# Optimization experiments

Hardware: AMD Instinct MI355X
Metric: run time of the kernel (lower is better)

## Reference

```python
import jax, jax.numpy as jnp
import numpy as np

EPS = 1e-5

def mvn(x):
    # instance norm with torch's unbiased variance (ddof=1), eps added to var
    b, c = x.shape[:2]
    flat = x.reshape(b, c, -1)
    mean = flat.mean(axis=2)[:, :, None, None]
    std = jnp.sqrt(flat.var(axis=2, ddof=1) + EPS)[:, :, None, None]
    return (x - mean) / std

def conv1x1(x, w, b):
    # w: [Cout, Cin], b: [Cout], x: [B, Cin, H, W]
    return jnp.einsum('oc,bchw->bohw', w, x) + b[None, :, None, None]

def setup_inputs() -> dict:
    key = jax.random.key(0)
    ks = jax.random.split(key, 20)
    B, C, H, W = 4, 512, 64, 64
    s = 1.0 / np.sqrt(C)  # kaiming-ish scale for stable softmax logits
    inp = {
        'content': jax.random.normal(ks[0], (B, C, H, W), jnp.float32),
        'style':   jax.random.normal(ks[1], (B, C, H, W), jnp.float32),
        'v_w':   jax.random.normal(ks[2], (C, C), jnp.float32) * s,
        'v_b':   jax.random.normal(ks[3], (C,), jnp.float32) * 0.01,
        'vsp_w': jax.random.normal(ks[4], (1, C), jnp.float32) * s,
        'vsp_b': jax.random.normal(ks[5], (1,), jnp.float32) * 0.01,
        'k_w':   jax.random.normal(ks[6], (C, C), jnp.float32) * s,
        'k_b':   jax.random.normal(ks[7], (C,), jnp.float32) * 0.01,
        'qg_w':  jax.random.normal(ks[8], (C, C), jnp.float32) * s,
        'qg_b':  jax.random.normal(ks[9], (C,), jnp.float32) * 0.01,
        'g1_w1': jax.random.normal(ks[10], (C, C), jnp.float32) * s,
        'g1_b1': jax.random.normal(ks[11], (C,), jnp.float32) * 0.01,
        'g1_w2': jax.random.normal(ks[12], (C, C), jnp.float32) * s,
        'g1_b2': jax.random.normal(ks[13], (C,), jnp.float32) * 0.01,
        'g2_w1': jax.random.normal(ks[14], (C, C), jnp.float32) * s,
        'g2_b1': jax.random.normal(ks[15], (C,), jnp.float32) * 0.01,
        'g2_w2': jax.random.normal(ks[16], (C, C), jnp.float32) * s,
        'g2_b2': jax.random.normal(ks[17], (C,), jnp.float32) * 0.01,
    }
    return inp

def reference(content, style, v_w, v_b, vsp_w, vsp_b, k_w, k_b, qg_w, qg_b,
              g1_w1, g1_b1, g1_w2, g1_b2, g2_w1, g2_b1, g2_w2, g2_b2):
    b, c, h_s, w_s = style.shape
    _, _, h_c, w_c = content.shape
    Ls, Lc = h_s * w_s, h_c * w_c

    V = conv1x1(style, v_w, v_b)                                  # [b,c,hs,ws]
    key_pool = conv1x1(mvn(style), vsp_w, vsp_b).reshape(b, 1, Ls)
    style_weights = jax.nn.softmax(key_pool, axis=-1)             # [b,1,Ls]
    # global style vector: V_flat @ weights^T -> [b,c,1]
    gsv = jnp.einsum('bcl,bl->bc', V.reshape(b, c, Ls), style_weights[:, 0, :])
    gsv4 = gsv[:, :, None, None]                                  # [b,c,1,1]

    Q_guide = conv1x1(mvn(content), qg_w, qg_b)                   # [b,c,hc,wc]
    gamma = conv1x1(jax.nn.relu(conv1x1(gsv4, g1_w1, g1_b1)), g1_w2, g1_b2)
    beta  = conv1x1(jax.nn.relu(conv1x1(gsv4, g2_w1, g2_b1)), g2_w2, g2_b2)
    local_guidance = gamma * Q_guide + beta                       # [b,c,hc,wc]

    Q = (Q_guide + local_guidance).reshape(b, c, Lc).transpose(0, 2, 1)  # [b,Lc,c]
    K = conv1x1(style, k_w, k_b).reshape(b, c, Ls)                       # [b,c,Ls]
    vv = V.reshape(b, c, Ls).transpose(0, 2, 1)                          # [b,Ls,c]

    energy = jnp.einsum('bqc,bck->bqk', Q, K)                     # [b,Lc,Ls]
    S = jax.nn.softmax(energy, axis=-1)
    out = jnp.einsum('bqk,bkc->bqc', S, vv)                       # [b,Lc,c]
    out = out.transpose(0, 2, 1).reshape(b, c, h_c, w_c)
    return mvn(content) + out
```

## Files before the change

kernel.cpp:

```cpp
#include <hip/hip_runtime.h>
#include <math.h>

typedef __bf16 bf16_t;
typedef _Float16 f16_t;
typedef __attribute__((ext_vector_type(8))) __bf16 bf16x8;
typedef __attribute__((ext_vector_type(8))) _Float16 f16x8;
typedef __attribute__((ext_vector_type(4))) float f32x4;

namespace {
constexpr int Bn = 4;
constexpr int Cn = 512;
constexpr int Ln = 4096;
constexpr float kEps = 1e-5f;
constexpr size_t NQK = (size_t)Bn * Ln * Cn;
constexpr size_t CC  = (size_t)Cn * Cn;

constexpr size_t FOFF_MEANS = 0;
constexpr size_t FOFF_RSTDS = 2048;
constexpr size_t FOFF_MEANC = 4096;
constexpr size_t FOFF_RSTDC = 6144;
constexpr size_t FOFF_KP    = 8192;
constexpr size_t FOFF_GSV   = FOFF_KP + 16384;
constexpr size_t FOFF_H1    = FOFF_GSV + 2048;
constexpr size_t FOFF_H2    = FOFF_H1 + 2048;
constexpr size_t FOFF_GAMMA = FOFF_H2 + 2048;
constexpr size_t FOFF_BETA  = FOFF_GAMMA + 2048;
}

__device__ inline f32x4 mfma_bf(bf16x8 a, bf16x8 b, f32x4 c) {
    return __builtin_amdgcn_mfma_f32_16x16x32_bf16(a, b, c, 0, 0, 0);
}
__device__ inline f32x4 mfma_f16(f16x8 a, f16x8 b, f32x4 c) {
    return __builtin_amdgcn_mfma_f32_16x16x32_f16(a, b, c, 0, 0, 0);
}

__device__ __forceinline__ void gll16(const void* g, void* l) {
    __builtin_amdgcn_global_load_lds((const unsigned int*)g, (unsigned int*)l, 16, 0, 0);
}

__device__ inline unsigned short h2u(f16_t x) {
    union { f16_t h; unsigned short u; } c; c.h = x; return c.u;
}
__device__ inline f16_t u2h(unsigned short x) {
    union { f16_t h; unsigned short u; } c; c.u = x; return c.h;
}

__global__ __launch_bounds__(256) void stats_kernel(const float* __restrict__ x,
                                                    float* __restrict__ mean,
                                                    float* __restrict__ rstd) {
    int bc = blockIdx.x;
    const float* row = x + (size_t)bc * Ln;
    float s1 = 0.f, s2 = 0.f;
    for (int i = threadIdx.x; i < Ln; i += 256) {
        float v = row[i];
        s1 += v; s2 += v * v;
    }
    for (int off = 32; off; off >>= 1) {
        s1 += __shfl_down(s1, off);
        s2 += __shfl_down(s2, off);
    }
    __shared__ float a1[4], a2[4];
    int wid = threadIdx.x >> 6;
    if ((threadIdx.x & 63) == 0) { a1[wid] = s1; a2[wid] = s2; }
    __syncthreads();
    if (threadIdx.x == 0) {
        s1 = a1[0] + a1[1] + a1[2] + a1[3];
        s2 = a2[0] + a2[1] + a2[2] + a2[3];
        float m = s1 / Ln;
        float var = (s2 - m * s1) / (Ln - 1);
        mean[bc] = m;
        rstd[bc] = 1.0f / sqrtf(var + kEps);
    }
}

__global__ __launch_bounds__(256) void split_w_kernel(const float* __restrict__ w0,
                                                      const float* __restrict__ w1,
                                                      const float* __restrict__ w2,
                                                      bf16_t* __restrict__ wsp) {
    const float* w = (blockIdx.y == 0) ? w0 : (blockIdx.y == 1) ? w1 : w2;
    bf16_t* hi = wsp + (size_t)blockIdx.y * 2 * CC;
    bf16_t* lo = hi + CC;
    size_t i0 = ((size_t)blockIdx.x * 256 + threadIdx.x) * 8;
    float4 a = *(const float4*)(w + i0);
    float4 b = *(const float4*)(w + i0 + 4);
    float vs[8] = {a.x, a.y, a.z, a.w, b.x, b.y, b.z, b.w};
    bf16x8 hv, lv;
#pragma unroll
    for (int i = 0; i < 8; i++) {
        bf16_t h = (bf16_t)vs[i];
        hv[i] = h;
        lv[i] = (bf16_t)(vs[i] - (float)h);
    }
    *(bf16x8*)(hi + i0) = hv;
    *(bf16x8*)(lo + i0) = lv;
}

template <bool MVN>
__global__ __launch_bounds__(256) void split_xt_kernel(const float* __restrict__ x,
                                                       const float* __restrict__ mean,
                                                       const float* __restrict__ rstd,
                                                       bf16_t* __restrict__ hi,
                                                       bf16_t* __restrict__ lo) {
    __shared__ bf16_t th[32][40];
    __shared__ bf16_t tl[32][40];
    int b = blockIdx.z, c0 = blockIdx.y * 32, l0 = blockIdx.x * 32;
    const size_t base = (size_t)b * Cn * Ln;
    int lc = threadIdx.x & 31;
    int cr0 = threadIdx.x >> 5;
#pragma unroll
    for (int p = 0; p < 4; p++) {
        int cr = cr0 + p * 8;
        float v = x[base + (size_t)(c0 + cr) * Ln + l0 + lc];
        if constexpr (MVN) {
            v = (v - mean[b * Cn + c0 + cr]) * rstd[b * Cn + c0 + cr];
        }
        bf16_t h = (bf16_t)v;
        th[lc][cr] = h;
        tl[lc][cr] = (bf16_t)(v - (float)h);
    }
    __syncthreads();
    int tt = threadIdx.x & 127;
    int lrow = tt >> 2;
    int c8 = (tt & 3) * 8;
    if (threadIdx.x < 128) {
        *(bf16x8*)(hi + base + (size_t)(l0 + lrow) * Cn + c0 + c8) = *(bf16x8*)&th[lrow][c8];
    } else {
        *(bf16x8*)(lo + base + (size_t)(l0 + lrow) * Cn + c0 + c8) = *(bf16x8*)&tl[lrow][c8];
    }
}

template <int MODE>
__global__ __launch_bounds__(256, 2) void conv_mfma_kernel(
    const bf16_t* __restrict__ Whi, const bf16_t* __restrict__ Wlo,
    const bf16_t* __restrict__ Xhi, const bf16_t* __restrict__ Xlo,
    const float* __restrict__ bias,
    const float* __restrict__ gma, const float* __restrict__ bta,
    f16_t* __restrict__ out0) {
    const int b = blockIdx.z;
    const int o0 = blockIdx.y * 128;
    const int l0 = blockIdx.x * 128;
    const int tid = threadIdx.x;
    const int lane = tid & 63, wid = tid >> 6;
    const int wm = wid & 1, wn = wid >> 1;
    const int lg = lane >> 4, li = lane & 15;
    const size_t bLC = (size_t)b * Ln * Cn;

    __shared__ __align__(16) char smem[66560];

    f32x4 acc[4][4];
#pragma unroll
    for (int i = 0; i < 4; i++)
#pragma unroll
        for (int j = 0; j < 4; j++) acc[i][j] = (f32x4){0.f, 0.f, 0.f, 0.f};

    for (int cc = 0; cc < Cn; cc += 64) {
        __syncthreads();
#pragma unroll
        for (int p = 0; p < 4; p++) {
            int idx = p * 256 + tid;
            int row = idx >> 3;
            int c8 = (idx & 7) * 8;
            unsigned off = (unsigned)((row * 64 + c8) * 2) ^ (unsigned)((row & 7) << 4);
            *(bf16x8*)(smem + off)         = *(const bf16x8*)(Whi + (size_t)(o0 + row) * Cn + cc + c8);
            *(bf16x8*)(smem + 16384 + off) = *(const bf16x8*)(Wlo + (size_t)(o0 + row) * Cn + cc + c8);
            *(bf16x8*)(smem + 32768 + off) = *(const bf16x8*)(Xhi + bLC + (size_t)(l0 + row) * Cn + cc + c8);
            *(bf16x8*)(smem + 49152 + off) = *(const bf16x8*)(Xlo + bLC + (size_t)(l0 + row) * Cn + cc + c8);
        }
        __syncthreads();
#pragma unroll
        for (int k2 = 0; k2 < 2; k2++) {
            bf16x8 ah[4], al[4], bh[4], bl[4];
#pragma unroll
            for (int f = 0; f < 4; f++) {
                int row = wm * 64 + f * 16 + li;
                unsigned ob = (unsigned)(row * 128 + ((k2 * 64 + lg * 16) ^ ((row & 7) << 4)));
                ah[f] = *(const bf16x8*)(smem + ob);
                al[f] = *(const bf16x8*)(smem + 16384 + ob);
            }
#pragma unroll
            for (int f = 0; f < 4; f++) {
                int row = wn * 64 + f * 16 + li;
                unsigned ob = (unsigned)(row * 128 + ((k2 * 64 + lg * 16) ^ ((row & 7) << 4)));
                bh[f] = *(const bf16x8*)(smem + 32768 + ob);
                bl[f] = *(const bf16x8*)(smem + 49152 + ob);
            }
#pragma unroll
            for (int fm = 0; fm < 4; fm++)
#pragma unroll
                for (int fn = 0; fn < 4; fn++) {
                    acc[fm][fn] = mfma_bf(ah[fm], bh[fn], acc[fm][fn]);
                    acc[fm][fn] = mfma_bf(ah[fm], bl[fn], acc[fm][fn]);
                    acc[fm][fn] = mfma_bf(al[fm], bh[fn], acc[fm][fn]);
                }
        }
    }

    if constexpr (MODE == 0) {
        const size_t bCL = (size_t)b * Cn * Ln;
#pragma unroll
        for (int fm = 0; fm < 4; fm++) {
#pragma unroll
            for (int r = 0; r < 4; r++) {
                int o = o0 + wm * 64 + fm * 16 + lg * 4 + r;
                float bv = bias[o];
#pragma unroll
                for (int fn = 0; fn < 4; fn++) {
                    int l = l0 + wn * 64 + fn * 16 + li;
                    out0[bCL + (size_t)o * Ln + l] = (f16_t)(acc[fm][fn][r] + bv);
                }
            }
        }
    } else {
        __syncthreads();
        unsigned short* ep = (unsigned short*)smem;
#pragma unroll
        for (int fm = 0; fm < 4; fm++) {
#pragma unroll
            for (int r = 0; r < 4; r++) {
                int orow = wm * 64 + fm * 16 + lg * 4 + r;
                int o = o0 + orow;
                float bv = bias[o];
                float gv = 0.f, btv = 0.f;
                if constexpr (MODE == 2) { gv = gma[b * Cn + o]; btv = bta[b * Cn + o]; }
#pragma unroll
                for (int fn = 0; fn < 4; fn++) {
                    int lrow = wn * 64 + fn * 16 + li;
                    float v = acc[fm][fn][r] + bv;
                    if constexpr (MODE == 2) v = v * (1.f + gv) + btv;
                    ep[lrow * 130 + orow] = h2u((f16_t)v);
                }
            }
        }
        __syncthreads();
#pragma unroll
        for (int p = 0; p < 8; p++) {
            int idx = p * 256 + tid;
            int lrow = idx >> 4;
            int c8 = (idx & 15) * 8;
            f16x8 hv;
#pragma unroll
            for (int u = 0; u < 8; u++) hv[u] = u2h(ep[lrow * 130 + c8 + u]);
            *(f16x8*)(out0 + bLC + (size_t)(l0 + lrow) * Cn + o0 + c8) = hv;
        }
    }
}

__global__ __launch_bounds__(256) void keypool_kernel(const float* __restrict__ style,
                                                      const float* __restrict__ vsp_w,
                                                      const float* __restrict__ vsp_b,
                                                      const float* __restrict__ mean_s,
                                                      const float* __restrict__ rstd_s,
                                                      float* __restrict__ kp) {
    int b = blockIdx.y;
    int l = blockIdx.x * 256 + threadIdx.x;
    const size_t bCL = (size_t)b * Cn * Ln;
    float acc = 0.f;
    for (int c = 0; c < Cn; c++) {
        float v = style[bCL + (size_t)c * Ln + l];
        acc += vsp_w[c] * (v - mean_s[b * Cn + c]) * rstd_s[b * Cn + c];
    }
    kp[b * Ln + l] = acc + vsp_b[0];
}

__global__ __launch_bounds__(1024) void softmax_kp_kernel(float* __restrict__ kp) {
    int b = blockIdx.x;
    float* p = kp + (size_t)b * Ln;
    int tid = threadIdx.x;
    float v[4];
    float m = -3e38f;
#pragma unroll
    for (int j = 0; j < 4; j++) { v[j] = p[tid + 1024 * j]; m = fmaxf(m, v[j]); }
    __shared__ float red[16];
    for (int off = 32; off; off >>= 1) m = fmaxf(m, __shfl_down(m, off));
    if ((tid & 63) == 0) red[tid >> 6] = m;
    __syncthreads();
    if (tid == 0) {
        float mm = red[0];
        for (int i = 1; i < 16; i++) mm = fmaxf(mm, red[i]);
        red[0] = mm;
    }
    __syncthreads();
    m = red[0];
    __syncthreads();
    float e[4]; float s = 0.f;
#pragma unroll
    for (int j = 0; j < 4; j++) { e[j] = __expf(v[j] - m); s += e[j]; }
    for (int off = 32; off; off >>= 1) s += __shfl_down(s, off);
    if ((tid & 63) == 0) red[tid >> 6] = s;
    __syncthreads();
    if (tid == 0) {
        float ss = 0.f;
        for (int i = 0; i < 16; i++) ss += red[i];
        red[0] = ss;
    }
    __syncthreads();
    float inv = 1.0f / red[0];
#pragma unroll
    for (int j = 0; j < 4; j++) p[tid + 1024 * j] = e[j] * inv;
}

__global__ __launch_bounds__(256) void gsv_kernel(const f16_t* __restrict__ Vf,
                                                  const float* __restrict__ w,
                                                  float* __restrict__ gsv) {
    int c = blockIdx.x, b = blockIdx.y;
    int tid = threadIdx.x;
    const f16_t* vp = Vf + ((size_t)b * Cn + c) * Ln;
    const float* wp = w + (size_t)b * Ln;
    float acc = 0.f;
    for (int base = tid * 8; base < Ln; base += 2048) {
        f16x8 v = *(const f16x8*)(vp + base);
        float4 w0 = *(const float4*)(wp + base);
        float4 w1 = *(const float4*)(wp + base + 4);
        acc += (float)v[0] * w0.x + (float)v[1] * w0.y + (float)v[2] * w0.z + (float)v[3] * w0.w;
        acc += (float)v[4] * w1.x + (float)v[5] * w1.y + (float)v[6] * w1.z + (float)v[7] * w1.w;
    }
    for (int off = 32; off; off >>= 1) acc += __shfl_down(acc, off);
    __shared__ float red[4];
    if ((tid & 63) == 0) red[tid >> 6] = acc;
    __syncthreads();
    if (tid == 0) gsv[(size_t)b * Cn + c] = red[0] + red[1] + red[2] + red[3];
}

__global__ __launch_bounds__(256) void mlp_hidden_kernel(const float* __restrict__ gsv,
                                                         const float* __restrict__ w1a, const float* __restrict__ b1a,
                                                         const float* __restrict__ w1b, const float* __restrict__ b1b,
                                                         float* __restrict__ h1, float* __restrict__ h2) {
    int idx = blockIdx.x * 256 + threadIdx.x;
    int b = idx / Cn, c = idx % Cn;
    float a1 = b1a[c], a2 = b1b[c];
    for (int k = 0; k < Cn; k++) {
        float g = gsv[b * Cn + k];
        a1 += w1a[(size_t)c * Cn + k] * g;
        a2 += w1b[(size_t)c * Cn + k] * g;
    }
    h1[idx] = fmaxf(a1, 0.f);
    h2[idx] = fmaxf(a2, 0.f);
}

__global__ __launch_bounds__(256) void mlp_out_kernel(const float* __restrict__ h1, const float* __restrict__ h2,
                                                      const float* __restrict__ w2a, const float* __restrict__ b2a,
                                                      const float* __restrict__ w2b, const float* __restrict__ b2b,
                                                      float* __restrict__ gamma, float* __restrict__ beta) {
    int idx = blockIdx.x * 256 + threadIdx.x;
    int b = idx / Cn, c = idx % Cn;
    float a1 = b2a[c], a2 = b2b[c];
    for (int k = 0; k < Cn; k++) {
        a1 += w2a[(size_t)c * Cn + k] * h1[b * Cn + k];
        a2 += w2b[(size_t)c * Cn + k] * h2[b * Cn + k];
    }
    gamma[idx] = a1;
    beta[idx] = a2;
}

__global__ __launch_bounds__(256, 2) void flash_kernel(
    const f16_t* __restrict__ Qf, const f16_t* __restrict__ Kf,
    const f16_t* __restrict__ Vf, float* __restrict__ Ot) {
    const int b = blockIdx.y;
    const int q0 = blockIdx.x * 32;
    const int tid = threadIdx.x;
    const int lane = tid & 63;
    const int wn = tid >> 6;
    const int lg = lane >> 4, li = lane & 15;

    __shared__ __align__(16) f16_t q_s[32 * 512];
    __shared__ __align__(16) f16_t kbuf[3 * 4096];
    __shared__ __align__(16) f16_t pb_s[32 * 64];
    __shared__ float smx[4][32];
    __shared__ float sml[4][32];

    const size_t qbase = ((size_t)b * Ln + q0) * Cn;
    const size_t kbase = (size_t)b * Ln * Cn;
    const size_t vbase = (size_t)b * Cn * Ln;

#pragma unroll
    for (int i = 0; i < 8; i++) {
        int idx = i * 256 + tid;
        int row = idx >> 6, slot = idx & 63;
        int sp = (slot & 56) | ((slot & 7) ^ (row & 7));
        gll16(Qf + qbase + (size_t)row * Cn + sp * 8, q_s + (size_t)idx * 8);
    }

    const int skey = tid >> 3;
    auto stageK = [&](int ktA, int cs, int bufi) {
#pragma unroll
        for (int i = 0; i < 2; i++) {
            int idx = i * 256 + tid;
            int key = idx >> 3, slot = idx & 7;
            int sp = slot ^ (key & 7);
            gll16(Kf + kbase + (size_t)(ktA + key) * Cn + cs * 64 + sp * 8,
                  kbuf + (size_t)bufi * 4096 + (size_t)idx * 8);
        }
        (void)skey;
    };

    stageK(0, 0, 0);
    stageK(0, 1, 1);
    __syncthreads();

    f32x4 o[2][8];
#pragma unroll
    for (int m = 0; m < 2; m++)
#pragma unroll
        for (int j = 0; j < 8; j++) o[m][j] = (f32x4){0.f, 0.f, 0.f, 0.f};
    float m_run[2][4], l_run[2][4];
#pragma unroll
    for (int m = 0; m < 2; m++)
#pragma unroll
        for (int r = 0; r < 4; r++) { m_run[m][r] = -1e30f; l_run[m][r] = 0.f; }

    const int key = wn * 16 + li;
    const unsigned kswz = (unsigned)((key & 7) << 4);

    for (int tile = 0; tile < 64; tile++) {
        const int kt = tile * 64;
        f32x4 e[2];
#pragma unroll
        for (int m = 0; m < 2; m++) e[m] = (f32x4){0.f, 0.f, 0.f, 0.f};

        for (int cs = 0; cs < 8; cs++) {
            const int cur = tile * 8 + cs;
            if (cur == 511) {
                asm volatile("s_waitcnt vmcnt(0)" ::: "memory");
            } else if (cur > 0) {
                asm volatile("s_waitcnt vmcnt(2)" ::: "memory");
            }
            asm volatile("s_barrier" ::: "memory");
            {
                int c2 = cur + 2;
                if (c2 < 512) stageK((c2 >> 3) << 6, c2 & 7, c2 % 3);
            }
            const char* kb = (const char*)kbuf + (cur % 3) * 8192;
#pragma unroll
            for (int k2 = 0; k2 < 2; k2++) {
                f16x8 bk = *(const f16x8*)(kb + key * 128 + ((k2 * 64 + lg * 16) ^ kswz));
                __builtin_amdgcn_s_setprio(1);
#pragma unroll
                for (int m = 0; m < 2; m++) {
                    int row = m * 16 + li;
                    f16x8 aq = *(const f16x8*)((const char*)q_s + row * 1024 +
                                ((cs * 128 + k2 * 64 + lg * 16) ^ ((row & 7) << 4)));
                    e[m] = mfma_f16(aq, bk, e[m]);
                }
                __builtin_amdgcn_s_setprio(0);
            }
        }

        float tmax[2][4];
#pragma unroll
        for (int m = 0; m < 2; m++)
#pragma unroll
            for (int r = 0; r < 4; r++) tmax[m][r] = e[m][r];
#pragma unroll
        for (int d = 1; d < 16; d <<= 1)
#pragma unroll
            for (int m = 0; m < 2; m++)
#pragma unroll
                for (int r = 0; r < 4; r++) tmax[m][r] = fmaxf(tmax[m][r], __shfl_xor(tmax[m][r], d));
        if (li == 0) {
#pragma unroll
            for (int m = 0; m < 2; m++)
#pragma unroll
                for (int r = 0; r < 4; r++) smx[wn][m * 16 + lg * 4 + r] = tmax[m][r];
        }
        asm volatile("s_waitcnt lgkmcnt(0)\n\ts_barrier" ::: "memory");
        float scv[2][4];
#pragma unroll
        for (int m = 0; m < 2; m++)
#pragma unroll
            for (int r = 0; r < 4; r++) {
                int row = m * 16 + lg * 4 + r;
                float tm = fmaxf(fmaxf(smx[0][row], smx[1][row]), fmaxf(smx[2][row], smx[3][row]));
                float mnew = fmaxf(m_run[m][r], tm);
                scv[m][r] = __expf(m_run[m][r] - mnew);
                m_run[m][r] = mnew;
            }
        float pv[2][4], rsum[2][4];
#pragma unroll
        for (int m = 0; m < 2; m++)
#pragma unroll
            for (int r = 0; r < 4; r++) {
                float pe = __expf(e[m][r] - m_run[m][r]);
                pv[m][r] = pe;
                rsum[m][r] = pe;
            }
#pragma unroll
        for (int d = 1; d < 16; d <<= 1)
#pragma unroll
            for (int m = 0; m < 2; m++)
#pragma unroll
                for (int r = 0; r < 4; r++) rsum[m][r] += __shfl_xor(rsum[m][r], d);
        if (li == 0) {
#pragma unroll
            for (int m = 0; m < 2; m++)
#pragma unroll
                for (int r = 0; r < 4; r++) sml[wn][m * 16 + lg * 4 + r] = rsum[m][r];
        }
#pragma unroll
        for (int m = 0; m < 2; m++)
#pragma unroll
            for (int r = 0; r < 4; r++) {
                int qrow = m * 16 + lg * 4 + r;
                unsigned boff = (unsigned)(qrow * 128 + ((2 * key) ^ ((qrow & 7) << 4)));
                *(f16_t*)((char*)pb_s + boff) = (f16_t)pv[m][r];
            }
#pragma unroll
        for (int m = 0; m < 2; m++)
#pragma unroll
            for (int j = 0; j < 8; j++)
#pragma unroll
                for (int r = 0; r < 4; r++) o[m][j][r] *= scv[m][r];
        asm volatile("s_waitcnt lgkmcnt(0)\n\ts_barrier" ::: "memory");
#pragma unroll
        for (int m = 0; m < 2; m++)
#pragma unroll
            for (int r = 0; r < 4; r++) {
                int row = m * 16 + lg * 4 + r;
                l_run[m][r] = l_run[m][r] * scv[m][r] + sml[0][row] + sml[1][row] + sml[2][row] + sml[3][row];
            }

        f16x8 pa[2][2];
#pragma unroll
        for (int m = 0; m < 2; m++)
#pragma unroll
            for (int k2 = 0; k2 < 2; k2++) {
                int qrow = m * 16 + li;
                pa[m][k2] = *(const f16x8*)((const char*)pb_s + qrow * 128 +
                              ((k2 * 64 + lg * 16) ^ ((qrow & 7) << 4)));
            }
        {
            const f16_t* vp0 = Vf + vbase + (size_t)(wn * 16 + li) * Ln + kt + lg * 8;
            f16x8 v0 = *(const f16x8*)(vp0);
            f16x8 v1 = *(const f16x8*)(vp0 + 32);
            for (int n = 0; n < 8; n++) {
                f16x8 n0 = v0, n1 = v1;
                if (n < 7) {
                    int cg = (n + 1) * 4 + wn;
                    const f16_t* vp = Vf + vbase + (size_t)(cg * 16 + li) * Ln + kt + lg * 8;
                    n0 = *(const f16x8*)(vp);
                    n1 = *(const f16x8*)(vp + 32);
                }
                __builtin_amdgcn_s_setprio(1);
#pragma unroll
                for (int m = 0; m < 2; m++) {
                    o[m][n] = mfma_f16(pa[m][0], v0, o[m][n]);
                    o[m][n] = mfma_f16(pa[m][1], v1, o[m][n]);
                }
                __builtin_amdgcn_s_setprio(0);
                v0 = n0; v1 = n1;
            }
        }
    }

#pragma unroll
    for (int m = 0; m < 2; m++)
#pragma unroll
        for (int r = 0; r < 4; r++) l_run[m][r] = 1.f / l_run[m][r];
#pragma unroll
    for (int m = 0; m < 2; m++)
#pragma unroll
        for (int n = 0; n < 8; n++) {
            int c = (n * 4 + wn) * 16 + li;
            int qg = q0 + m * 16 + lg * 4;
            float4 ov;
            ov.x = o[m][n][0] * l_run[m][0];
            ov.y = o[m][n][1] * l_run[m][1];
            ov.z = o[m][n][2] * l_run[m][2];
            ov.w = o[m][n][3] * l_run[m][3];
            *(float4*)(Ot + vbase + (size_t)c * Ln + qg) = ov;
        }
}

__global__ __launch_bounds__(256) void final_kernel(const float* __restrict__ content,
                                                    const float* __restrict__ mean_c,
                                                    const float* __restrict__ rstd_c,
                                                    float* __restrict__ out) {
    size_t gid = (size_t)blockIdx.x * 256 + threadIdx.x;
    size_t linear = gid * 4;
    int ch = (int)(linear / Ln);
    float m = mean_c[ch], rs = rstd_c[ch];
    float4 cv = *(const float4*)(content + linear);
    float4 ov = *(const float4*)(out + linear);
    ov.x += (cv.x - m) * rs;
    ov.y += (cv.y - m) * rs;
    ov.z += (cv.z - m) * rs;
    ov.w += (cv.w - m) * rs;
    *(float4*)(out + linear) = ov;
}

extern "C" void kernel_launch(void* const* d_in, const int* in_sizes, int n_in,
                              void* d_out, int out_size, void* d_ws, size_t ws_size,
                              hipStream_t stream) {
    const float* content = (const float*)d_in[0];
    const float* style   = (const float*)d_in[1];
    const float* v_w   = (const float*)d_in[2];
    const float* v_b   = (const float*)d_in[3];
    const float* vsp_w = (const float*)d_in[4];
    const float* vsp_b = (const float*)d_in[5];
    const float* k_w   = (const float*)d_in[6];
    const float* k_b   = (const float*)d_in[7];
    const float* qg_w  = (const float*)d_in[8];
    const float* qg_b  = (const float*)d_in[9];
    const float* g1_w1 = (const float*)d_in[10];
    const float* g1_b1 = (const float*)d_in[11];
    const float* g1_w2 = (const float*)d_in[12];
    const float* g1_b2 = (const float*)d_in[13];
    const float* g2_w1 = (const float*)d_in[14];
    const float* g2_b1 = (const float*)d_in[15];
    const float* g2_w2 = (const float*)d_in[16];
    const float* g2_b2 = (const float*)d_in[17];

    f16_t* wsh = (f16_t*)d_ws;
    f16_t* Qf = wsh;
    f16_t* Kf = wsh + NQK;
    f16_t* Vf = wsh + 2 * NQK;
    bf16_t* wsp = (bf16_t*)(wsh + 3 * NQK);
    bf16_t* Wv_hi = wsp;            bf16_t* Wv_lo = wsp + CC;
    bf16_t* Wk_hi = wsp + 2 * CC;   bf16_t* Wk_lo = wsp + 3 * CC;
    bf16_t* Wq_hi = wsp + 4 * CC;   bf16_t* Wq_lo = wsp + 5 * CC;

    float* wsf = (float*)(wsp + 6 * CC);
    float* mean_s = wsf + FOFF_MEANS;
    float* rstd_s = wsf + FOFF_RSTDS;
    float* mean_c = wsf + FOFF_MEANC;
    float* rstd_c = wsf + FOFF_RSTDC;
    float* kp     = wsf + FOFF_KP;
    float* gsv    = wsf + FOFF_GSV;
    float* h1     = wsf + FOFF_H1;
    float* h2     = wsf + FOFF_H2;
    float* gamma  = wsf + FOFF_GAMMA;
    float* beta   = wsf + FOFF_BETA;

    bf16_t* XThi = (bf16_t*)d_out;
    bf16_t* XTlo = XThi + NQK;
    float* outF  = (float*)d_out;

    stats_kernel<<<dim3(Bn * Cn), 256, 0, stream>>>(style, mean_s, rstd_s);
    stats_kernel<<<dim3(Bn * Cn), 256, 0, stream>>>(content, mean_c, rstd_c);

    split_w_kernel<<<dim3(CC / 2048, 3), 256, 0, stream>>>(v_w, k_w, qg_w, wsp);
    split_xt_kernel<false><<<dim3(Ln / 32, Cn / 32, Bn), 256, 0, stream>>>(style, nullptr, nullptr, XThi, XTlo);

    dim3 cgrid(Ln / 128, Cn / 128, Bn);
    conv_mfma_kernel<0><<<cgrid, 256, 0, stream>>>(Wv_hi, Wv_lo, XThi, XTlo, v_b, nullptr, nullptr, Vf);

    keypool_kernel<<<dim3(Ln / 256, Bn), 256, 0, stream>>>(style, vsp_w, vsp_b, mean_s, rstd_s, kp);
    softmax_kp_kernel<<<dim3(Bn), 1024, 0, stream>>>(kp);
    gsv_kernel<<<dim3(Cn, Bn), 256, 0, stream>>>(Vf, kp, gsv);
    mlp_hidden_kernel<<<dim3(Bn * Cn / 256), 256, 0, stream>>>(gsv, g1_w1, g1_b1, g2_w1, g2_b1, h1, h2);
    mlp_out_kernel<<<dim3(Bn * Cn / 256), 256, 0, stream>>>(h1, h2, g1_w2, g1_b2, g2_w2, g2_b2, gamma, beta);

    conv_mfma_kernel<1><<<cgrid, 256, 0, stream>>>(Wk_hi, Wk_lo, XThi, XTlo, k_b, nullptr, nullptr, Kf);

    split_xt_kernel<true><<<dim3(Ln / 32, Cn / 32, Bn), 256, 0, stream>>>(content, mean_c, rstd_c, XThi, XTlo);
    conv_mfma_kernel<2><<<cgrid, 256, 0, stream>>>(Wq_hi, Wq_lo, XThi, XTlo, qg_b, gamma, beta, Qf);

    flash_kernel<<<dim3(Ln / 32, Bn), 256, 0, stream>>>(Qf, Kf, Vf, outF);

    final_kernel<<<dim3((Bn * Cn * (Ln / 4)) / 256), 256, 0, stream>>>(content, mean_c, rstd_c, outF);
}
```

Before: 772.2 us.

## Hold Q in registers, deepen K pipeline, prefetch V earlier, remap blocks to XCDs

```diff
diff --git a/kernel.cpp b/kernel.cpp
--- a/kernel.cpp
+++ b/kernel.cpp
@@ -355,15 +355,17 @@
 __global__ __launch_bounds__(256, 2) void flash_kernel(
     const f16_t* __restrict__ Qf, const f16_t* __restrict__ Kf,
     const f16_t* __restrict__ Vf, float* __restrict__ Ot) {
-    const int b = blockIdx.y;
-    const int q0 = blockIdx.x * 32;
+    const int bid = blockIdx.x;
+    const int wgid = (bid & 7) * 64 + (bid >> 3);
+    const int b = wgid >> 7;
+    const int q0 = (wgid & 127) * 32;
+
     const int tid = threadIdx.x;
     const int lane = tid & 63;
     const int wn = tid >> 6;
     const int lg = lane >> 4, li = lane & 15;
 
-    __shared__ __align__(16) f16_t q_s[32 * 512];
-    __shared__ __align__(16) f16_t kbuf[3 * 4096];
+    __shared__ __align__(16) f16_t kbuf[4 * 4096];
     __shared__ __align__(16) f16_t pb_s[32 * 64];
     __shared__ float smx[4][32];
     __shared__ float sml[4][32];
@@ -372,15 +374,16 @@
     const size_t kbase = (size_t)b * Ln * Cn;
     const size_t vbase = (size_t)b * Cn * Ln;
 
-#pragma unroll
-    for (int i = 0; i < 8; i++) {
-        int idx = i * 256 + tid;
-        int row = idx >> 6, slot = idx & 63;
-        int sp = (slot & 56) | ((slot & 7) ^ (row & 7));
-        gll16(Qf + qbase + (size_t)row * Cn + sp * 8, q_s + (size_t)idx * 8);
-    }
-
-    const int skey = tid >> 3;
+    f16x8 qf[2][8][2];
+#pragma unroll
+    for (int m = 0; m < 2; m++)
+#pragma unroll
+        for (int cs = 0; cs < 8; cs++)
+#pragma unroll
+            for (int k2 = 0; k2 < 2; k2++)
+                qf[m][cs][k2] = *(const f16x8*)(Qf + qbase + (size_t)(m * 16 + li) * Cn +
+                                                cs * 64 + k2 * 32 + lg * 8);
+
     auto stageK = [&](int ktA, int cs, int bufi) {
 #pragma unroll
         for (int i = 0; i < 2; i++) {
@@ -390,12 +393,11 @@
             gll16(Kf + kbase + (size_t)(ktA + key) * Cn + cs * 64 + sp * 8,
                   kbuf + (size_t)bufi * 4096 + (size_t)idx * 8);
         }
-        (void)skey;
     };
 
     stageK(0, 0, 0);
     stageK(0, 1, 1);
-    __syncthreads();
+    stageK(0, 2, 2);
 
     f32x4 o[2][8];
 #pragma unroll
@@ -417,32 +419,41 @@
 #pragma unroll
         for (int m = 0; m < 2; m++) e[m] = (f32x4){0.f, 0.f, 0.f, 0.f};
 
+#pragma unroll
         for (int cs = 0; cs < 8; cs++) {
             const int cur = tile * 8 + cs;
-            if (cur == 511) {
+            if (cur < 510) {
+                asm volatile("s_waitcnt vmcnt(4)" ::: "memory");
+            } else if (cur == 510) {
+                asm volatile("s_waitcnt vmcnt(2)" ::: "memory");
+            } else {
                 asm volatile("s_waitcnt vmcnt(0)" ::: "memory");
-            } else if (cur > 0) {
-                asm volatile("s_waitcnt vmcnt(2)" ::: "memory");
             }
             asm volatile("s_barrier" ::: "memory");
             {
-                int c2 = cur + 2;
-                if (c2 < 512) stageK((c2 >> 3) << 6, c2 & 7, c2 % 3);
-            }
-            const char* kb = (const char*)kbuf + (cur % 3) * 8192;
+                int c3 = cur + 3;
+                if (c3 < 512) stageK((c3 >> 3) << 6, c3 & 7, c3 & 3);
+            }
+            const char* kb = (const char*)kbuf + (cur & 3) * 8192;
 #pragma unroll
             for (int k2 = 0; k2 < 2; k2++) {
                 f16x8 bk = *(const f16x8*)(kb + key * 128 + ((k2 * 64 + lg * 16) ^ kswz));
                 __builtin_amdgcn_s_setprio(1);
 #pragma unroll
-                for (int m = 0; m < 2; m++) {
-                    int row = m * 16 + li;
-                    f16x8 aq = *(const f16x8*)((const char*)q_s + row * 1024 +
-                                ((cs * 128 + k2 * 64 + lg * 16) ^ ((row & 7) << 4)));
-                    e[m] = mfma_f16(aq, bk, e[m]);
-                }
+                for (int m = 0; m < 2; m++)
+                    e[m] = mfma_f16(qf[m][cs][k2], bk, e[m]);
                 __builtin_amdgcn_s_setprio(0);
             }
+        }
+
+        f16x8 va[2], vb[2];
+        {
+            const f16_t* vp0 = Vf + vbase + (size_t)(0 * 4 + wn) * 16 * Ln + (size_t)li * Ln + kt + lg * 8;
+            va[0] = *(const f16x8*)(vp0);
+            vb[0] = *(const f16x8*)(vp0 + 32);
+            const f16_t* vp1 = Vf + vbase + (size_t)(1 * 4 + wn) * 16 * Ln + (size_t)li * Ln + kt + lg * 8;
+            va[1] = *(const f16x8*)(vp1);
+            vb[1] = *(const f16x8*)(vp1 + 32);
         }
 
         float tmax[2][4];
@@ -464,6 +475,7 @@
         }
         asm volatile("s_waitcnt lgkmcnt(0)\n\ts_barrier" ::: "memory");
         float scv[2][4];
+        bool anyresc = false;
 #pragma unroll
         for (int m = 0; m < 2; m++)
 #pragma unroll
@@ -472,6 +484,7 @@
                 float tm = fmaxf(fmaxf(smx[0][row], smx[1][row]), fmaxf(smx[2][row], smx[3][row]));
                 float mnew = fmaxf(m_run[m][r], tm);
                 scv[m][r] = __expf(m_run[m][r] - mnew);
+                anyresc |= (mnew > m_run[m][r]);
                 m_run[m][r] = mnew;
             }
         float pv[2][4], rsum[2][4];
@@ -503,12 +516,14 @@
                 unsigned boff = (unsigned)(qrow * 128 + ((2 * key) ^ ((qrow & 7) << 4)));
                 *(f16_t*)((char*)pb_s + boff) = (f16_t)pv[m][r];
             }
-#pragma unroll
-        for (int m = 0; m < 2; m++)
-#pragma unroll
-            for (int j = 0; j < 8; j++)
-#pragma unroll
-                for (int r = 0; r < 4; r++) o[m][j][r] *= scv[m][r];
+        if (__any((int)anyresc)) {
+#pragma unroll
+            for (int m = 0; m < 2; m++)
+#pragma unroll
+                for (int j = 0; j < 8; j++)
+#pragma unroll
+                    for (int r = 0; r < 4; r++) o[m][j][r] *= scv[m][r];
+        }
         asm volatile("s_waitcnt lgkmcnt(0)\n\ts_barrier" ::: "memory");
 #pragma unroll
         for (int m = 0; m < 2; m++)
@@ -527,27 +542,23 @@
                 pa[m][k2] = *(const f16x8*)((const char*)pb_s + qrow * 128 +
                               ((k2 * 64 + lg * 16) ^ ((qrow & 7) << 4)));
             }
-        {
-            const f16_t* vp0 = Vf + vbase + (size_t)(wn * 16 + li) * Ln + kt + lg * 8;
-            f16x8 v0 = *(const f16x8*)(vp0);
-            f16x8 v1 = *(const f16x8*)(vp0 + 32);
-            for (int n = 0; n < 8; n++) {
-                f16x8 n0 = v0, n1 = v1;
-                if (n < 7) {
-                    int cg = (n + 1) * 4 + wn;
-                    const f16_t* vp = Vf + vbase + (size_t)(cg * 16 + li) * Ln + kt + lg * 8;
-                    n0 = *(const f16x8*)(vp);
-                    n1 = *(const f16x8*)(vp + 32);
-                }
-                __builtin_amdgcn_s_setprio(1);
-#pragma unroll
-                for (int m = 0; m < 2; m++) {
-                    o[m][n] = mfma_f16(pa[m][0], v0, o[m][n]);
-                    o[m][n] = mfma_f16(pa[m][1], v1, o[m][n]);
-                }
-                __builtin_amdgcn_s_setprio(0);
-                v0 = n0; v1 = n1;
-            }
+#pragma unroll
+        for (int n = 0; n < 8; n++) {
+            const int slot = n & 1;
+            f16x8 c0 = va[slot], c1 = vb[slot];
+            if (n + 2 < 8) {
+                int cg = (n + 2) * 4 + wn;
+                const f16_t* vp = Vf + vbase + (size_t)(cg * 16 + li) * Ln + kt + lg * 8;
+                va[slot] = *(const f16x8*)(vp);
+                vb[slot] = *(const f16x8*)(vp + 32);
+            }
+            __builtin_amdgcn_s_setprio(1);
+#pragma unroll
+            for (int m = 0; m < 2; m++) {
+                o[m][n] = mfma_f16(pa[m][0], c0, o[m][n]);
+                o[m][n] = mfma_f16(pa[m][1], c1, o[m][n]);
+            }
+            __builtin_amdgcn_s_setprio(0);
         }
     }
 
@@ -654,7 +665,7 @@
     split_xt_kernel<true><<<dim3(Ln / 32, Cn / 32, Bn), 256, 0, stream>>>(content, mean_c, rstd_c, XThi, XTlo);
     conv_mfma_kernel<2><<<cgrid, 256, 0, stream>>>(Wq_hi, Wq_lo, XThi, XTlo, qg_b, gamma, beta, Qf);
 
-    flash_kernel<<<dim3(Ln / 32, Bn), 256, 0, stream>>>(Qf, Kf, Vf, outF);
+    flash_kernel<<<dim3((Ln / 32) * Bn), 256, 0, stream>>>(Qf, Kf, Vf, outF);
 
     final_kernel<<<dim3((Bn * Cn * (Ln / 4)) / 256), 256, 0, stream>>>(content, mean_c, rstd_c, outF);
 }
```

After: 1.284 ms. 1.66x slower.
